# Performance work log

Hardware: AMD Instinct MI355X
Metric: run time of the kernel (lower is better)

The kernel has to match this reference:

```python
import jax, jax.numpy as jnp
import numpy as np

B, S, H, U = 32, 2048, 1024, 1024


def setup_inputs() -> dict:
    key = jax.random.key(0)
    ks = jax.random.split(key, 5)
    sc = 1.0 / np.sqrt(H)
    return {
        "hidden_t": jax.random.normal(ks[0], (B, H), jnp.float32),
        "hiddens": jax.random.normal(ks[1], (B, S, H), jnp.float32),
        "W1": jax.random.normal(ks[2], (H, U), jnp.float32) * sc,
        "b1": jnp.zeros((U,), jnp.float32),
        "W2": jax.random.normal(ks[3], (H, U), jnp.float32) * sc,
        "b2": jnp.zeros((U,), jnp.float32),
        "V": jax.random.normal(ks[4], (U, 1), jnp.float32) * sc,
        "bV": jnp.zeros((1,), jnp.float32),
    }


def reference(hidden_t, hiddens, W1, b1, W2, b2, V, bV):
    # proj of encoder states: [B,S,U]; proj of decoder state broadcast over time: [B,1,U]
    keys = jnp.einsum("bsh,hu->bsu", hiddens, W1) + b1
    query = (hidden_t @ W2 + b2)[:, None, :]
    score = jnp.tanh(keys + query) @ V + bV            # [B,S,1]
    attention_weights = jax.nn.softmax(score, axis=1)  # softmax over seq axis
    context_vector = jnp.sum(attention_weights * hiddens, axis=1)  # [B,H]
    return context_vector, attention_weights
```

## Files before the change

### kernel.cpp

```cpp
#include <hip/hip_runtime.h>
#include <hip/hip_bf16.h>
#include <cstdint>

#define S_LEN 2048
#define B_SZ  32
#define H_DIM 1024
#define U_DIM 1024

#define BM 128
#define BN 128
#define BK 32
#define LDT 40

using short8  = __attribute__((ext_vector_type(8))) short;
using floatx4 = __attribute__((ext_vector_type(4))) float;

typedef __attribute__((address_space(3))) void lds_void;
typedef const __attribute__((address_space(1))) void glb_void;
#define GLD16(g, s) __builtin_amdgcn_global_load_lds((glb_void*)(g), (lds_void*)(s), 16, 0, 0)

__device__ __forceinline__ unsigned short f32_to_bf16_rne(float f) {
    unsigned int u = __float_as_uint(f);
    unsigned int r = (u + 0x7fffu + ((u >> 16) & 1u)) >> 16;
    return (unsigned short)r;
}

__global__ __launch_bounds__(256)
void cast_hiddens_kernel(const float* __restrict__ src, unsigned short* __restrict__ dst) {
    const size_t i = ((size_t)blockIdx.x * 256 + threadIdx.x) * 8;
    float4 a = *(const float4*)(src + i);
    float4 b = *(const float4*)(src + i + 4);
    ushort4 lo, hi;
    lo.x = f32_to_bf16_rne(a.x); lo.y = f32_to_bf16_rne(a.y);
    lo.z = f32_to_bf16_rne(a.z); lo.w = f32_to_bf16_rne(a.w);
    hi.x = f32_to_bf16_rne(b.x); hi.y = f32_to_bf16_rne(b.y);
    hi.z = f32_to_bf16_rne(b.z); hi.w = f32_to_bf16_rne(b.w);
    *(ushort4*)(dst + i)     = lo;
    *(ushort4*)(dst + i + 4) = hi;
}

__global__ void transpose_cast_w1(const float* __restrict__ W1,
                                  unsigned short* __restrict__ W1t) {
    __shared__ float tile[32][33];
    const int tx = threadIdx.x, ty = threadIdx.y;
    const int u0 = blockIdx.x * 32, h0 = blockIdx.y * 32;
#pragma unroll
    for (int i = 0; i < 4; ++i)
        tile[ty * 4 + i][tx] = W1[(size_t)(h0 + ty * 4 + i) * U_DIM + u0 + tx];
    __syncthreads();
#pragma unroll
    for (int i = 0; i < 4; ++i)
        W1t[(size_t)(u0 + ty * 4 + i) * H_DIM + h0 + tx] =
            f32_to_bf16_rne(tile[tx][ty * 4 + i]);
}

__global__ void query_kernel(const float* __restrict__ hidden_t,
                             const float* __restrict__ W2,
                             const float* __restrict__ b1,
                             const float* __restrict__ b2,
                             float* __restrict__ query) {
    const int b = blockIdx.y;
    const int u = blockIdx.x * 128 + threadIdx.x;
    const float* ht = hidden_t + b * H_DIM;
    float acc = b1[u] + b2[u];
#pragma unroll 8
    for (int h = 0; h < H_DIM; ++h)
        acc = fmaf(ht[h], W2[(size_t)h * U_DIM + u], acc);
    query[b * U_DIM + u] = acc;
}

__device__ __forceinline__ void score_epilogue(const floatx4 acc[4][4],
                                               const float* __restrict__ qrow,
                                               const float* __restrict__ V,
                                               float* __restrict__ scores,
                                               int m0, int n0, int wr, int wc, int q, int r) {
#pragma unroll
    for (int mt = 0; mt < 4; ++mt) {
#pragma unroll
        for (int reg = 0; reg < 4; ++reg) {
            float sum = 0.f;
#pragma unroll
            for (int nt = 0; nt < 4; ++nt) {
                const int c = n0 + wc * 64 + nt * 16 + r;
                float x = acc[mt][nt][reg] + qrow[c];
                x = fminf(fmaxf(x, -15.f), 15.f);
                float e = __expf(2.f * x);
                float t = (e - 1.f) / (e + 1.f);
                sum = fmaf(t, V[c], sum);
            }
            sum += __shfl_xor(sum, 1);
            sum += __shfl_xor(sum, 2);
            sum += __shfl_xor(sum, 4);
            sum += __shfl_xor(sum, 8);
            if (r == 0)
                atomicAdd(&scores[m0 + wr * 64 + mt * 16 + q * 4 + reg], sum);
        }
    }
}

__global__ __launch_bounds__(256)
void keys_score_v2(const unsigned short* __restrict__ hb,
                   const unsigned short* __restrict__ W1t,
                   const float* __restrict__ query,
                   const float* __restrict__ V,
                   float* __restrict__ scores) {
    __shared__ unsigned short As[BM * BK];
    __shared__ unsigned short Bs[BN * BK];

    const int tid = threadIdx.x;
    const int w = tid >> 6, l = tid & 63;
    const int q = l >> 4, r = l & 15;
    const int wr = w >> 1, wc = w & 1;
    const int m0 = blockIdx.y * BM;
    const int n0 = blockIdx.x * BN;

    const int srow   = l >> 2;
    const int schunk = (l & 3) * 8;

    const unsigned short* gA0 = hb  + ((size_t)(m0 + w * 32 +  0 + srow) << 10) + schunk;
    const unsigned short* gA1 = hb  + ((size_t)(m0 + w * 32 + 16 + srow) << 10) + schunk;
    const unsigned short* gB0 = W1t + ((size_t)(n0 + w * 32 +  0 + srow) << 10) + schunk;
    const unsigned short* gB1 = W1t + ((size_t)(n0 + w * 32 + 16 + srow) << 10) + schunk;

    floatx4 acc[4][4];
#pragma unroll
    for (int mt = 0; mt < 4; ++mt)
#pragma unroll
        for (int nt = 0; nt < 4; ++nt)
            acc[mt][nt] = (floatx4){0.f, 0.f, 0.f, 0.f};

    for (int kt = 0; kt < H_DIM / BK; ++kt) {
        GLD16(gA0, &As[(w * 2 + 0) * 512]);
        GLD16(gA1, &As[(w * 2 + 1) * 512]);
        GLD16(gB0, &Bs[(w * 2 + 0) * 512]);
        GLD16(gB1, &Bs[(w * 2 + 1) * 512]);
        gA0 += BK; gA1 += BK; gB0 += BK; gB1 += BK;

        __syncthreads();

        short8 af[4], bfr[4];
#pragma unroll
        for (int mt = 0; mt < 4; ++mt)
            af[mt] = *(const short8*)&As[(wr * 64 + mt * 16 + r) * BK + q * 8];
#pragma unroll
        for (int nt = 0; nt < 4; ++nt)
            bfr[nt] = *(const short8*)&Bs[(wc * 64 + nt * 16 + r) * BK + q * 8];
#pragma unroll
        for (int mt = 0; mt < 4; ++mt)
#pragma unroll
            for (int nt = 0; nt < 4; ++nt)
                acc[mt][nt] = __builtin_amdgcn_mfma_f32_16x16x32_bf16(
                    af[mt], bfr[nt], acc[mt][nt], 0, 0, 0);

        __syncthreads();
    }

    const float* qrow = query + (m0 >> 11) * U_DIM;
    score_epilogue(acc, qrow, V, scores, m0, n0, wr, wc, q, r);
}

__global__ __launch_bounds__(256)
void keys_score_v1(const float* __restrict__ hiddens,
                   const unsigned short* __restrict__ W1t,
                   const float* __restrict__ query,
                   const float* __restrict__ V,
                   float* __restrict__ scores) {
    __shared__ unsigned short As[BM][LDT];
    __shared__ unsigned short Bs[BN][LDT];

    const int tid = threadIdx.x;
    const int lane = tid & 63, wave = tid >> 6;
    const int q = lane >> 4, r = lane & 15;
    const int wr = wave >> 1, wc = wave & 1;
    const int m0 = blockIdx.y * BM, n0 = blockIdx.x * BN;
    const int arow = tid >> 3, achunk = tid & 7;
    const int brow = tid >> 2, bchunk = tid & 3;

    floatx4 acc[4][4];
#pragma unroll
    for (int mt = 0; mt < 4; ++mt)
#pragma unroll
        for (int nt = 0; nt < 4; ++nt)
            acc[mt][nt] = (floatx4){0.f, 0.f, 0.f, 0.f};

    for (int kt = 0; kt < H_DIM / BK; ++kt) {
        const float* ag = hiddens + (size_t)(m0 + arow) * H_DIM + kt * BK + achunk * 4;
#pragma unroll
        for (int i = 0; i < 4; ++i) {
            float4 f = *(const float4*)(ag + (size_t)i * 32 * H_DIM);
            ushort4 h;
            h.x = f32_to_bf16_rne(f.x); h.y = f32_to_bf16_rne(f.y);
            h.z = f32_to_bf16_rne(f.z); h.w = f32_to_bf16_rne(f.w);
            *(ushort4*)&As[arow + i * 32][achunk * 4] = h;
        }
        const unsigned short* bg = W1t + (size_t)(n0 + brow) * H_DIM + kt * BK + bchunk * 8;
#pragma unroll
        for (int i = 0; i < 2; ++i)
            *(uint4*)&Bs[brow + i * 64][bchunk * 8] = *(const uint4*)(bg + (size_t)i * 64 * H_DIM);
        __syncthreads();
        short8 af[4], bfr[4];
#pragma unroll
        for (int mt = 0; mt < 4; ++mt)
            af[mt] = *(const short8*)&As[wr * 64 + mt * 16 + r][q * 8];
#pragma unroll
        for (int nt = 0; nt < 4; ++nt)
            bfr[nt] = *(const short8*)&Bs[wc * 64 + nt * 16 + r][q * 8];
#pragma unroll
        for (int mt = 0; mt < 4; ++mt)
#pragma unroll
            for (int nt = 0; nt < 4; ++nt)
                acc[mt][nt] = __builtin_amdgcn_mfma_f32_16x16x32_bf16(
                    af[mt], bfr[nt], acc[mt][nt], 0, 0, 0);
        __syncthreads();
    }
    const float* qrow = query + (m0 >> 11) * U_DIM;
    score_epilogue(acc, qrow, V, scores, m0, n0, wr, wc, q, r);
}

__global__ void softmax_kernel(const float* __restrict__ scores,
                               float* __restrict__ wout) {
    const int b = blockIdx.x, tid = threadIdx.x;
    const int wave = tid >> 6, lane = tid & 63;
    const float* src = scores + b * S_LEN;
    float v[8];
    float m = -1e30f;
#pragma unroll
    for (int i = 0; i < 8; ++i) { v[i] = src[tid + i * 256]; m = fmaxf(m, v[i]); }
#pragma unroll
    for (int off = 32; off >= 1; off >>= 1) m = fmaxf(m, __shfl_xor(m, off));
    __shared__ float red[4];
    if (lane == 0) red[wave] = m;
    __syncthreads();
    m = fmaxf(fmaxf(red[0], red[1]), fmaxf(red[2], red[3]));
    __syncthreads();
    float s = 0.f;
#pragma unroll
    for (int i = 0; i < 8; ++i) { v[i] = __expf(v[i] - m); s += v[i]; }
#pragma unroll
    for (int off = 32; off >= 1; off >>= 1) s += __shfl_xor(s, off);
    if (lane == 0) red[wave] = s;
    __syncthreads();
    s = red[0] + red[1] + red[2] + red[3];
    const float inv = 1.f / s;
#pragma unroll
    for (int i = 0; i < 8; ++i) wout[b * S_LEN + tid + i * 256] = v[i] * inv;
}

__global__ __launch_bounds__(256)
void context_kernel(const float* __restrict__ weights,
                    const float* __restrict__ hiddens,
                    float* __restrict__ out_ctx) {
    const int b = blockIdx.y;
    const int sc = blockIdx.x;
    const int h4 = threadIdx.x * 4;
    const float* wrow = weights + b * S_LEN + sc * 128;
    const float* hbase = hiddens + ((size_t)b * S_LEN + sc * 128) * H_DIM + h4;
    float4 acc = make_float4(0.f, 0.f, 0.f, 0.f);
    for (int s = 0; s < 128; ++s) {
        const float w = wrow[s];
        float4 hv = *(const float4*)(hbase + (size_t)s * H_DIM);
        acc.x = fmaf(w, hv.x, acc.x);
        acc.y = fmaf(w, hv.y, acc.y);
        acc.z = fmaf(w, hv.z, acc.z);
        acc.w = fmaf(w, hv.w, acc.w);
    }
    float* o = out_ctx + b * H_DIM + h4;
    atomicAdd(o + 0, acc.x);
    atomicAdd(o + 1, acc.y);
    atomicAdd(o + 2, acc.z);
    atomicAdd(o + 3, acc.w);
}

extern "C" void kernel_launch(void* const* d_in, const int* in_sizes, int n_in,
                              void* d_out, int out_size, void* d_ws, size_t ws_size,
                              hipStream_t stream) {
    const float* hidden_t = (const float*)d_in[0];
    const float* hiddens  = (const float*)d_in[1];
    const float* W1       = (const float*)d_in[2];
    const float* b1       = (const float*)d_in[3];
    const float* W2       = (const float*)d_in[4];
    const float* b2       = (const float*)d_in[5];
    const float* V        = (const float*)d_in[6];

    float* out_ctx = (float*)d_out;
    float* out_w   = (float*)d_out + B_SZ * H_DIM;

    char* ws = (char*)d_ws;
    unsigned short* W1t = (unsigned short*)ws;
    float* query  = (float*)(ws + (2u << 20));
    float* scores = query + B_SZ * U_DIM;
    unsigned short* hb = (unsigned short*)(ws + (4u << 20));
    const size_t need = (4u << 20) + (size_t)B_SZ * S_LEN * H_DIM * 2;

    hipMemsetAsync(scores, 0, (size_t)B_SZ * S_LEN * sizeof(float), stream);
    hipMemsetAsync(out_ctx, 0, (size_t)B_SZ * H_DIM * sizeof(float), stream);

    transpose_cast_w1<<<dim3(32, 32), dim3(32, 8), 0, stream>>>(W1, W1t);
    query_kernel<<<dim3(8, B_SZ), 128, 0, stream>>>(hidden_t, W2, b1, b2, query);

    if (ws_size >= need) {
        cast_hiddens_kernel<<<32768, 256, 0, stream>>>(hiddens, hb);
        keys_score_v2<<<dim3(U_DIM / BN, (B_SZ * S_LEN) / BM), 256, 0, stream>>>(
            hb, W1t, query, V, scores);
    } else {
        keys_score_v1<<<dim3(U_DIM / BN, (B_SZ * S_LEN) / BM), 256, 0, stream>>>(
            hiddens, W1t, query, V, scores);
    }

    softmax_kernel<<<B_SZ, 256, 0, stream>>>(scores, out_w);
    context_kernel<<<dim3(S_LEN / 128, B_SZ), 256, 0, stream>>>(out_w, hiddens, out_ctx);
}
```

Baseline: 713.0 us.

## Double GEMM K-tile, swizzle block order for L2 reuse, split context more finely

The bf16 keys GEMM now stages a 64-wide K slice per iteration, loaded with eight direct global-to-LDS copies per thread, which halves the number of barrier pairs per output tile. Blocks use a 1D grid remapped so that groups of 8 row bands sweep all 8 column tiles together, improving L2 reuse of the hiddens rows. The context reduction uses 64-row chunks instead of 128 for more parallel blocks, at the cost of twice as many atomics. The larger LDS tile and unpadded layout may raise LDS bank conflicts and reduce occupancy.

After: 746.0 us. +4.6%, slower.

```diff
diff --git a/kernel.cpp b/kernel.cpp
--- a/kernel.cpp
+++ b/kernel.cpp
@@ -9,8 +9,7 @@
 
 #define BM 128
 #define BN 128
-#define BK 32
-#define LDT 40
+#define BK 64
 
 using short8  = __attribute__((ext_vector_type(8))) short;
 using floatx4 = __attribute__((ext_vector_type(4))) float;
@@ -99,7 +98,7 @@
 }
 
 __global__ __launch_bounds__(256)
-void keys_score_v2(const unsigned short* __restrict__ hb,
+void keys_score_v3(const unsigned short* __restrict__ hb,
                    const unsigned short* __restrict__ W1t,
                    const float* __restrict__ query,
                    const float* __restrict__ V,
@@ -111,16 +110,20 @@
     const int w = tid >> 6, l = tid & 63;
     const int q = l >> 4, r = l & 15;
     const int wr = w >> 1, wc = w & 1;
-    const int m0 = blockIdx.y * BM;
-    const int n0 = blockIdx.x * BN;
-
-    const int srow   = l >> 2;
-    const int schunk = (l & 3) * 8;
-
-    const unsigned short* gA0 = hb  + ((size_t)(m0 + w * 32 +  0 + srow) << 10) + schunk;
-    const unsigned short* gA1 = hb  + ((size_t)(m0 + w * 32 + 16 + srow) << 10) + schunk;
-    const unsigned short* gB0 = W1t + ((size_t)(n0 + w * 32 +  0 + srow) << 10) + schunk;
-    const unsigned short* gB1 = W1t + ((size_t)(n0 + w * 32 + 16 + srow) << 10) + schunk;
+
+    const int bid = blockIdx.x;
+    const int col      = (bid >> 3) & 7;
+    const int row_band = ((bid >> 6) << 3) | (bid & 7);
+    const int m0 = row_band * BM;
+    const int n0 = col * BN;
+
+    const int srow   = l >> 3;
+    const int schunk = (l & 7) * 8;
+
+    const unsigned short* gA = hb  + ((size_t)(m0 + w * 8 + srow) << 10) + schunk;
+    const unsigned short* gB = W1t + ((size_t)(n0 + w * 8 + srow) << 10) + schunk;
+    unsigned short* lA = &As[(w * 8) * BK];
+    unsigned short* lB = &Bs[(w * 8) * BK];
 
     floatx4 acc[4][4];
 #pragma unroll
@@ -130,27 +133,31 @@
             acc[mt][nt] = (floatx4){0.f, 0.f, 0.f, 0.f};
 
     for (int kt = 0; kt < H_DIM / BK; ++kt) {
-        GLD16(gA0, &As[(w * 2 + 0) * 512]);
-        GLD16(gA1, &As[(w * 2 + 1) * 512]);
-        GLD16(gB0, &Bs[(w * 2 + 0) * 512]);
-        GLD16(gB1, &Bs[(w * 2 + 1) * 512]);
-        gA0 += BK; gA1 += BK; gB0 += BK; gB1 += BK;
+#pragma unroll
+        for (int i = 0; i < 4; ++i) {
+            GLD16(gA + ((size_t)(i * 32) << 10), lA + i * 32 * BK);
+            GLD16(gB + ((size_t)(i * 32) << 10), lB + i * 32 * BK);
+        }
+        gA += BK; gB += BK;
 
         __syncthreads();
 
-        short8 af[4], bfr[4];
-#pragma unroll
-        for (int mt = 0; mt < 4; ++mt)
-            af[mt] = *(const short8*)&As[(wr * 64 + mt * 16 + r) * BK + q * 8];
-#pragma unroll
-        for (int nt = 0; nt < 4; ++nt)
-            bfr[nt] = *(const short8*)&Bs[(wc * 64 + nt * 16 + r) * BK + q * 8];
-#pragma unroll
-        for (int mt = 0; mt < 4; ++mt)
+#pragma unroll
+        for (int kh = 0; kh < 2; ++kh) {
+            short8 af[4], bfr[4];
+#pragma unroll
+            for (int mt = 0; mt < 4; ++mt)
+                af[mt] = *(const short8*)&As[(wr * 64 + mt * 16 + r) * BK + kh * 32 + q * 8];
 #pragma unroll
             for (int nt = 0; nt < 4; ++nt)
-                acc[mt][nt] = __builtin_amdgcn_mfma_f32_16x16x32_bf16(
-                    af[mt], bfr[nt], acc[mt][nt], 0, 0, 0);
+                bfr[nt] = *(const short8*)&Bs[(wc * 64 + nt * 16 + r) * BK + kh * 32 + q * 8];
+#pragma unroll
+            for (int mt = 0; mt < 4; ++mt)
+#pragma unroll
+                for (int nt = 0; nt < 4; ++nt)
+                    acc[mt][nt] = __builtin_amdgcn_mfma_f32_16x16x32_bf16(
+                        af[mt], bfr[nt], acc[mt][nt], 0, 0, 0);
+        }
 
         __syncthreads();
     }
@@ -165,9 +172,8 @@
                    const float* __restrict__ query,
                    const float* __restrict__ V,
                    float* __restrict__ scores) {
-    __shared__ unsigned short As[BM][LDT];
-    __shared__ unsigned short Bs[BN][LDT];
-
+    __shared__ unsigned short As[BM][40];
+    __shared__ unsigned short Bs[BN][40];
     const int tid = threadIdx.x;
     const int lane = tid & 63, wave = tid >> 6;
     const int q = lane >> 4, r = lane & 15;
@@ -175,16 +181,14 @@
     const int m0 = blockIdx.y * BM, n0 = blockIdx.x * BN;
     const int arow = tid >> 3, achunk = tid & 7;
     const int brow = tid >> 2, bchunk = tid & 3;
-
     floatx4 acc[4][4];
 #pragma unroll
     for (int mt = 0; mt < 4; ++mt)
 #pragma unroll
         for (int nt = 0; nt < 4; ++nt)
             acc[mt][nt] = (floatx4){0.f, 0.f, 0.f, 0.f};
-
-    for (int kt = 0; kt < H_DIM / BK; ++kt) {
-        const float* ag = hiddens + (size_t)(m0 + arow) * H_DIM + kt * BK + achunk * 4;
+    for (int kt = 0; kt < H_DIM / 32; ++kt) {
+        const float* ag = hiddens + (size_t)(m0 + arow) * H_DIM + kt * 32 + achunk * 4;
 #pragma unroll
         for (int i = 0; i < 4; ++i) {
             float4 f = *(const float4*)(ag + (size_t)i * 32 * H_DIM);
@@ -193,7 +197,7 @@
             h.z = f32_to_bf16_rne(f.z); h.w = f32_to_bf16_rne(f.w);
             *(ushort4*)&As[arow + i * 32][achunk * 4] = h;
         }
-        const unsigned short* bg = W1t + (size_t)(n0 + brow) * H_DIM + kt * BK + bchunk * 8;
+        const unsigned short* bg = W1t + (size_t)(n0 + brow) * H_DIM + kt * 32 + bchunk * 8;
 #pragma unroll
         for (int i = 0; i < 2; ++i)
             *(uint4*)&Bs[brow + i * 64][bchunk * 8] = *(const uint4*)(bg + (size_t)i * 64 * H_DIM);
@@ -253,10 +257,10 @@
     const int b = blockIdx.y;
     const int sc = blockIdx.x;
     const int h4 = threadIdx.x * 4;
-    const float* wrow = weights + b * S_LEN + sc * 128;
-    const float* hbase = hiddens + ((size_t)b * S_LEN + sc * 128) * H_DIM + h4;
+    const float* wrow = weights + b * S_LEN + sc * 64;
+    const float* hbase = hiddens + ((size_t)b * S_LEN + sc * 64) * H_DIM + h4;
     float4 acc = make_float4(0.f, 0.f, 0.f, 0.f);
-    for (int s = 0; s < 128; ++s) {
+    for (int s = 0; s < 64; ++s) {
         const float w = wrow[s];
         float4 hv = *(const float4*)(hbase + (size_t)s * H_DIM);
         acc.x = fmaf(w, hv.x, acc.x);
@@ -300,13 +304,13 @@
 
     if (ws_size >= need) {
         cast_hiddens_kernel<<<32768, 256, 0, stream>>>(hiddens, hb);
-        keys_score_v2<<<dim3(U_DIM / BN, (B_SZ * S_LEN) / BM), 256, 0, stream>>>(
+        keys_score_v3<<<(U_DIM / BN) * ((B_SZ * S_LEN) / BM), 256, 0, stream>>>(
             hb, W1t, query, V, scores);
     } else {
-        keys_score_v1<<<dim3(U_DIM / BN, (B_SZ * S_LEN) / BM), 256, 0, stream>>>(
+        keys_score_v1<<<dim3(U_DIM / 128, (B_SZ * S_LEN) / BM), 256, 0, stream>>>(
             hiddens, W1t, query, V, scores);
     }
 
     softmax_kernel<<<B_SZ, 256, 0, stream>>>(scores, out_w);
-    context_kernel<<<dim3(S_LEN / 128, B_SZ), 256, 0, stream>>>(out_w, hiddens, out_ctx);
-}
+    context_kernel<<<dim3(S_LEN / 64, B_SZ), 256, 0, stream>>>(out_w, hiddens, out_ctx);
+}
```
